# Kernel tuning notes

Measured on AMD Instinct MI355X. Metric: run time of the kernel, lower is better.

The kernel has to match this reference:

```python
import jax, jax.numpy as jnp
import numpy as np

TEMPERATURE = 0.1
NEG_INF = -1e30


def setup_inputs() -> dict:
    key = jax.random.key(0)
    ks = jax.random.split(key, 8)
    T, B, D = 2048, 16, 256
    inp = {
        'q1': jax.random.normal(ks[0], (T, B, D), dtype=jnp.float32),
        'k2': jax.random.normal(ks[1], (T, B, D), dtype=jnp.float32),
        'q2': jax.random.normal(ks[2], (T, B, D), dtype=jnp.float32),
        'k1': jax.random.normal(ks[3], (T, B, D), dtype=jnp.float32),
        'mask_q1': jnp.ones((B, T), dtype=bool),
        'mask_q2': jnp.ones((B, T), dtype=bool),
        'len_q1': jax.random.randint(ks[4], (B,), 0, T, dtype=jnp.int32),
        'len_k2': jax.random.randint(ks[5], (B,), 0, T, dtype=jnp.int32),
        'len_q2': jax.random.randint(ks[6], (B,), 0, T, dtype=jnp.int32),
        'len_k1': jax.random.randint(ks[7], (B,), 0, T, dtype=jnp.int32),
    }
    return inp


def _compute_loss(pred, target, len_pred, len_target):
    # pred, target: (T, B, D) -> (B, T, D)
    pred = jnp.transpose(pred, (1, 0, 2))
    target = jnp.transpose(target, (1, 0, 2))
    B, T, _ = pred.shape
    min_l = jnp.minimum(len_pred, len_target)  # (B,)

    # Batched truncated matmul realized as full matmul + column masking.
    logits = jnp.einsum('btd,bsd->bts', pred, target) / TEMPERATURE  # (B, T, T)
    idx = jnp.arange(T)
    col_valid = idx[None, None, :] < min_l[:, None, None]
    logits = jnp.where(col_valid, logits, NEG_INF)

    # Cross-entropy with labels = arange(min_l): loss_i = lse_i - logits[i, i]
    lse = jax.nn.logsumexp(logits, axis=-1)                 # (B, T)
    diag = jnp.diagonal(logits, axis1=1, axis2=2)           # (B, T)
    row_loss = lse - diag

    row_valid = idx[None, :] < min_l[:, None]               # (B, T)
    denom = jnp.maximum(min_l, 1).astype(pred.dtype)
    per_sample = jnp.sum(jnp.where(row_valid, row_loss, 0.0), axis=1) / denom

    valid = min_l > 0
    n_valid = jnp.sum(valid.astype(pred.dtype))
    total = jnp.sum(jnp.where(valid, per_sample, 0.0))
    return jnp.where(n_valid > 0, total / jnp.maximum(n_valid, 1.0), 0.0)


def reference(q1, k2, q2, k1, mask_q1, mask_q2, len_q1, len_k2, len_q2, len_k1):
    # masks are unused in the original math (kept for interface fidelity)
    loss_a = _compute_loss(q1, k2, len_q1, len_k2)
    loss_b = _compute_loss(q2, k1, len_q2, len_k1)
    return (loss_a + loss_b) / 2
```

## Files before the change

### kernel.cpp

```cpp
#include <hip/hip_runtime.h>
#include <hip/hip_bf16.h>
#include <cmath>

#define T_DIM 2048
#define B_DIM 16
#define D_DIM 256
#define BD (B_DIM * D_DIM)
#define BM 256
#define BN 64
#define NS 4
#define CHUNK (T_DIM / NS)
#define NEG_INF_F (-1e30f)

typedef __attribute__((ext_vector_type(8))) short bf16x8;
typedef __attribute__((ext_vector_type(8))) unsigned short ushort8;
typedef __attribute__((ext_vector_type(4))) float f32x4;

static __device__ __forceinline__ ushort f2bf(float f) {
    union { float f; unsigned int u; } x; x.f = f;
    unsigned int r = (x.u + 0x7FFFu + ((x.u >> 16) & 1u)) >> 16;
    return (ushort)r;
}

static __device__ __forceinline__ void gload_lds16(const ushort* g, ushort* l) {
    __builtin_amdgcn_global_load_lds(
        (const __attribute__((address_space(1))) unsigned int*)g,
        (__attribute__((address_space(3))) unsigned int*)l,
        16, 0, 0);
}

__global__ __launch_bounds__(256) void convert_kernel(
    const float* __restrict__ q1, const float* __restrict__ k2,
    const float* __restrict__ q2, const float* __restrict__ k1,
    const int* __restrict__ lq1, const int* __restrict__ lk2,
    const int* __restrict__ lq2, const int* __restrict__ lk1,
    ushort* __restrict__ wsbf)
{
    const int idx    = blockIdx.x * 256 + threadIdx.x;
    const int tensor = idx >> 20;
    const int rem    = idx & 1048575;
    const int t      = rem >> 9;
    const int r2     = rem & 511;
    const int b      = r2 >> 5;
    const int d8     = (r2 & 31) * 8;
    const int m = (tensor < 2) ? min(lq1[b], lk2[b]) : min(lq2[b], lk1[b]);
    if (t >= m) return;

    const float* src = (tensor == 0) ? q1 : (tensor == 1) ? k2 : (tensor == 2) ? q2 : k1;
    const float scale = (tensor == 0 || tensor == 2) ? 10.0f : 1.0f;
    const size_t off = (size_t)t * BD + (size_t)b * D_DIM + d8;
    const float4 v0 = *reinterpret_cast<const float4*>(&src[off]);
    const float4 v1 = *reinterpret_cast<const float4*>(&src[off + 4]);
    ushort8 h;
    h[0] = f2bf(v0.x * scale); h[1] = f2bf(v0.y * scale);
    h[2] = f2bf(v0.z * scale); h[3] = f2bf(v0.w * scale);
    h[4] = f2bf(v1.x * scale); h[5] = f2bf(v1.y * scale);
    h[6] = f2bf(v1.z * scale); h[7] = f2bf(v1.w * scale);
    const size_t TBD = (size_t)T_DIM * BD;
    ushort* dst = &wsbf[(size_t)tensor * TBD + (size_t)t * BD + (size_t)b * D_DIM
                        + (d8 ^ ((t & 15) << 3))];
    *reinterpret_cast<ushort8*>(dst) = h;
}

__global__ __launch_bounds__(512) void partial_lse_bf_kernel(
    const ushort* __restrict__ wsbf,
    const int* __restrict__ len_q1, const int* __restrict__ len_k2,
    const int* __restrict__ len_q2, const int* __restrict__ len_k1,
    float2* __restrict__ partial, float* __restrict__ diag)
{
    const int pair = blockIdx.z / NS;
    const int sc   = blockIdx.z % NS;
    const int b    = blockIdx.y;
    const int t0   = blockIdx.x * BM;

    const int lp = (pair == 0) ? len_q1[b] : len_q2[b];
    const int lt = (pair == 0) ? len_k2[b] : len_k1[b];
    const int m  = min(lp, lt);
    const int s_start = sc * CHUNK;
    if (t0 >= m || s_start >= m) return;
    const int s_hi = min(m, s_start + CHUNK);
    const int pb = pair * B_DIM + b;

    const size_t TBD = (size_t)T_DIM * BD;
    const ushort* pred = wsbf + (size_t)(pair ? 2 : 0) * TBD;
    const ushort* targ = wsbf + (size_t)(pair ? 3 : 1) * TBD;

    __shared__ ushort tl[2][BN * 256];

    const int tid = threadIdx.x;
    const int w   = tid >> 6;
    const int l   = tid & 63;
    const int c   = l & 15;
    const int g   = l >> 4;

    #pragma unroll
    for (int q = 0; q < 4; ++q) {
        const int r = 8 * w + 2 * q + (l >> 5);
        const ushort* gp = &targ[(size_t)(s_start + r) * BD + (size_t)b * D_DIM + (l & 31) * 8];
        gload_lds16(gp, &tl[0][(4 * w + q) * 512]);
    }

    bf16x8 afrag[2][8];
    #pragma unroll
    for (int i = 0; i < 2; ++i) {
        const ushort* base = &pred[(size_t)(t0 + 32 * w + 16 * i + c) * BD + (size_t)b * D_DIM];
        #pragma unroll
        for (int kk = 0; kk < 8; ++kk) {
            const int d = g * 8 + kk * 32;
            afrag[i][kk] = *reinterpret_cast<const bf16x8*>(&base[d ^ (c << 3)]);
        }
    }

    float tmax[2][4], tsum[2][4], dg[2][4];
    #pragma unroll
    for (int i = 0; i < 2; ++i)
        #pragma unroll
        for (int rr = 0; rr < 4; ++rr) {
            tmax[i][rr] = NEG_INF_F; tsum[i][rr] = 0.0f; dg[i][rr] = NEG_INF_F;
        }

    __syncthreads();
    int cur = 0;

    for (int s0 = s_start; s0 < s_hi; s0 += BN) {
        if (s0 + BN < s_hi) {
            const int nxt = cur ^ 1;
            #pragma unroll
            for (int q = 0; q < 4; ++q) {
                const int r = 8 * w + 2 * q + (l >> 5);
                const ushort* gp = &targ[(size_t)(s0 + BN + r) * BD + (size_t)b * D_DIM + (l & 31) * 8];
                gload_lds16(gp, &tl[nxt][(4 * w + q) * 512]);
            }
        }

        f32x4 acc[2][4];
        #pragma unroll
        for (int i = 0; i < 2; ++i)
            #pragma unroll
            for (int j = 0; j < 4; ++j)
                acc[i][j] = (f32x4){0.f, 0.f, 0.f, 0.f};

        const ushort* buf = tl[cur];
        #pragma unroll
        for (int kk = 0; kk < 8; ++kk) {
            bf16x8 bfrag[4];
            #pragma unroll
            for (int j = 0; j < 4; ++j) {
                const int r = 16 * j + c;
                const int d = g * 8 + kk * 32;
                bfrag[j] = *reinterpret_cast<const bf16x8*>(&buf[(r << 8) + (d ^ (c << 3))]);
            }
            #pragma unroll
            for (int i = 0; i < 2; ++i)
                #pragma unroll
                for (int j = 0; j < 4; ++j)
                    acc[i][j] = __builtin_amdgcn_mfma_f32_16x16x32_bf16(
                        afrag[i][kk], bfrag[j], acc[i][j], 0, 0, 0);
        }

        #pragma unroll
        for (int i = 0; i < 2; ++i) {
            #pragma unroll
            for (int rr = 0; rr < 4; ++rr) {
                const int trow = t0 + 32 * w + 16 * i + 4 * g + rr;
                float lg[4];
                float cmax = NEG_INF_F;
                #pragma unroll
                for (int j = 0; j < 4; ++j) {
                    const int s = s0 + 16 * j + c;
                    float v = acc[i][j][rr];
                    v = (s < m) ? v : NEG_INF_F;
                    if (s == trow) dg[i][rr] = v;
                    lg[j] = v;
                    cmax = fmaxf(cmax, v);
                }
                const float nmax = fmaxf(tmax[i][rr], cmax);
                const float add = __expf(lg[0] - nmax) + __expf(lg[1] - nmax)
                                + __expf(lg[2] - nmax) + __expf(lg[3] - nmax);
                tsum[i][rr] = tsum[i][rr] * __expf(tmax[i][rr] - nmax) + add;
                tmax[i][rr] = nmax;
            }
        }

        __syncthreads();
        cur ^= 1;
    }

    const bool own_diag = (t0 >= s_start) && (t0 + BM <= s_start + CHUNK);
    #pragma unroll
    for (int i = 0; i < 2; ++i) {
        #pragma unroll
        for (int rr = 0; rr < 4; ++rr) {
            float M = tmax[i][rr], S = tsum[i][rr];
            #pragma unroll
            for (int msk = 1; msk < 16; msk <<= 1) {
                const float Mo = __shfl_xor(M, msk, 64);
                const float So = __shfl_xor(S, msk, 64);
                const float nM = fmaxf(M, Mo);
                S = S * __expf(M - nM) + So * __expf(Mo - nM);
                M = nM;
            }
            float d = dg[i][rr];
            #pragma unroll
            for (int msk = 1; msk < 16; msk <<= 1)
                d = fmaxf(d, __shfl_xor(d, msk, 64));
            if (c == 0) {
                const int trow = t0 + 32 * w + 16 * i + 4 * g + rr;
                partial[((size_t)(pb << 11) + trow) * NS + sc] = make_float2(M, S);
                if (own_diag) diag[(pb << 11) + trow] = d;
            }
        }
    }
}

__global__ __launch_bounds__(256) void partial_lse_f32_kernel(
    const float* __restrict__ q1, const float* __restrict__ k2,
    const float* __restrict__ q2, const float* __restrict__ k1,
    const int* __restrict__ len_q1, const int* __restrict__ len_k2,
    const int* __restrict__ len_q2, const int* __restrict__ len_k1,
    float2* __restrict__ partial, float* __restrict__ diag,
    int chunk, int ns)
{
    const int pair = blockIdx.z / ns;
    const int sc   = blockIdx.z % ns;
    const int b    = blockIdx.y;
    const int t0   = blockIdx.x * 128;

    const float* pred = (pair == 0) ? q1 : q2;
    const float* targ = (pair == 0) ? k2 : k1;
    const int lp = (pair == 0) ? len_q1[b] : len_q2[b];
    const int lt = (pair == 0) ? len_k2[b] : len_k1[b];
    const int m  = min(lp, lt);
    const int s_start = sc * chunk;
    if (t0 >= m || s_start >= m) return;
    const int s_hi = min(m, s_start + chunk);
    const int pb = pair * B_DIM + b;

    __shared__ ushort tlf[BN * 256];

    const int tid = threadIdx.x;
    const int w   = tid >> 6;
    const int l   = tid & 63;
    const int c   = l & 15;
    const int g   = l >> 4;

    bf16x8 afrag[2][8];
    #pragma unroll
    for (int i = 0; i < 2; ++i) {
        const float* base = &pred[(size_t)(t0 + 32 * w + 16 * i + c) * BD + (size_t)b * D_DIM];
        #pragma unroll
        for (int kk = 0; kk < 8; ++kk) {
            const int d = g * 8 + kk * 32;
            const float4 v0 = *reinterpret_cast<const float4*>(base + d);
            const float4 v1 = *reinterpret_cast<const float4*>(base + d + 4);
            bf16x8 av;
            av[0] = (short)f2bf(v0.x * 10.f); av[1] = (short)f2bf(v0.y * 10.f);
            av[2] = (short)f2bf(v0.z * 10.f); av[3] = (short)f2bf(v0.w * 10.f);
            av[4] = (short)f2bf(v1.x * 10.f); av[5] = (short)f2bf(v1.y * 10.f);
            av[6] = (short)f2bf(v1.z * 10.f); av[7] = (short)f2bf(v1.w * 10.f);
            afrag[i][kk] = av;
        }
    }

    float tmax[2][4], tsum[2][4], dg[2][4];
    #pragma unroll
    for (int i = 0; i < 2; ++i)
        #pragma unroll
        for (int rr = 0; rr < 4; ++rr) {
            tmax[i][rr] = NEG_INF_F; tsum[i][rr] = 0.0f; dg[i][rr] = NEG_INF_F;
        }

    for (int s0 = s_start; s0 < s_hi; s0 += BN) {
        __syncthreads();
        #pragma unroll
        for (int v = 0; v < 16; ++v) {
            const int f  = v * 256 + tid;
            const int r  = f >> 6;
            const int d0 = (f & 63) * 4;
            const float4 vv = *reinterpret_cast<const float4*>(
                &targ[(size_t)(s0 + r) * BD + (size_t)b * D_DIM + d0]);
            ushort4 h;
            h.x = f2bf(vv.x); h.y = f2bf(vv.y); h.z = f2bf(vv.z); h.w = f2bf(vv.w);
            *reinterpret_cast<ushort4*>(&tlf[(r << 8) + (d0 ^ ((r & 15) << 3))]) = h;
        }
        __syncthreads();

        f32x4 acc[2][4];
        #pragma unroll
        for (int i = 0; i < 2; ++i)
            #pragma unroll
            for (int j = 0; j < 4; ++j)
                acc[i][j] = (f32x4){0.f, 0.f, 0.f, 0.f};

        #pragma unroll
        for (int kk = 0; kk < 8; ++kk) {
            bf16x8 bfrag[4];
            #pragma unroll
            for (int j = 0; j < 4; ++j) {
                const int r = 16 * j + c;
                const int d = g * 8 + kk * 32;
                bfrag[j] = *reinterpret_cast<const bf16x8*>(&tlf[(r << 8) + (d ^ (c << 3))]);
            }
            #pragma unroll
            for (int i = 0; i < 2; ++i)
                #pragma unroll
                for (int j = 0; j < 4; ++j)
                    acc[i][j] = __builtin_amdgcn_mfma_f32_16x16x32_bf16(
                        afrag[i][kk], bfrag[j], acc[i][j], 0, 0, 0);
        }

        #pragma unroll
        for (int i = 0; i < 2; ++i) {
            #pragma unroll
            for (int rr = 0; rr < 4; ++rr) {
                const int trow = t0 + 32 * w + 16 * i + 4 * g + rr;
                float lg[4];
                float cmax = NEG_INF_F;
                #pragma unroll
                for (int j = 0; j < 4; ++j) {
                    const int s = s0 + 16 * j + c;
                    float v = acc[i][j][rr];
                    v = (s < m) ? v : NEG_INF_F;
                    if (s == trow) dg[i][rr] = v;
                    lg[j] = v;
                    cmax = fmaxf(cmax, v);
                }
                const float nmax = fmaxf(tmax[i][rr], cmax);
                const float add = __expf(lg[0] - nmax) + __expf(lg[1] - nmax)
                                + __expf(lg[2] - nmax) + __expf(lg[3] - nmax);
                tsum[i][rr] = tsum[i][rr] * __expf(tmax[i][rr] - nmax) + add;
                tmax[i][rr] = nmax;
            }
        }
    }

    const bool own_diag = (t0 >= s_start) && (t0 + 128 <= s_start + chunk);
    #pragma unroll
    for (int i = 0; i < 2; ++i) {
        #pragma unroll
        for (int rr = 0; rr < 4; ++rr) {
            float M = tmax[i][rr], S = tsum[i][rr];
            #pragma unroll
            for (int msk = 1; msk < 16; msk <<= 1) {
                const float Mo = __shfl_xor(M, msk, 64);
                const float So = __shfl_xor(S, msk, 64);
                const float nM = fmaxf(M, Mo);
                S = S * __expf(M - nM) + So * __expf(Mo - nM);
                M = nM;
            }
            float d = dg[i][rr];
            #pragma unroll
            for (int msk = 1; msk < 16; msk <<= 1)
                d = fmaxf(d, __shfl_xor(d, msk, 64));
            if (c == 0) {
                const int trow = t0 + 32 * w + 16 * i + 4 * g + rr;
                partial[((size_t)(pb << 11) + trow) * ns + sc] = make_float2(M, S);
                if (own_diag) diag[(pb << 11) + trow] = d;
            }
        }
    }
}

__global__ __launch_bounds__(256) void combine_kernel(
    const int* __restrict__ len_q1, const int* __restrict__ len_k2,
    const int* __restrict__ len_q2, const int* __restrict__ len_k1,
    const float2* __restrict__ partial, const float* __restrict__ diag,
    float* __restrict__ per_sample, int chunk, int ns)
{
    const int pb   = blockIdx.x;
    const int pair = pb >> 4;
    const int b    = pb & 15;
    const int lp = (pair == 0) ? len_q1[b] : len_q2[b];
    const int lt = (pair == 0) ? len_k2[b] : len_k1[b];
    const int m  = min(lp, lt);

    float local = 0.0f;
    if (m > 0) {
        const int nch = (m + chunk - 1) / chunk;
        for (int t = threadIdx.x; t < m; t += 256) {
            float M = NEG_INF_F, S = 0.0f;
            for (int sc = 0; sc < nch; ++sc) {
                const float2 p = partial[((size_t)(pb << 11) + t) * ns + sc];
                const float nM = fmaxf(M, p.x);
                S = S * __expf(M - nM) + p.y * __expf(p.x - nM);
                M = nM;
            }
            local += (__logf(S) + M) - diag[(pb << 11) + t];
        }
    }

    __shared__ float ws4[4];
    #pragma unroll
    for (int msk = 1; msk < 64; msk <<= 1)
        local += __shfl_xor(local, msk, 64);
    if ((threadIdx.x & 63) == 0) ws4[threadIdx.x >> 6] = local;
    __syncthreads();
    if (threadIdx.x == 0) {
        const float tot = ws4[0] + ws4[1] + ws4[2] + ws4[3];
        per_sample[pb] = (m > 0) ? (tot / (float)m) : 0.0f;
    }
}

__global__ void finalize_kernel(
    const int* __restrict__ len_q1, const int* __restrict__ len_k2,
    const int* __restrict__ len_q2, const int* __restrict__ len_k1,
    const float* __restrict__ per_sample, float* __restrict__ out)
{
    if (threadIdx.x != 0 || blockIdx.x != 0) return;
    float losses[2];
    #pragma unroll
    for (int p = 0; p < 2; ++p) {
        float tot = 0.0f, nv = 0.0f;
        for (int b = 0; b < B_DIM; ++b) {
            const int lp = (p == 0) ? len_q1[b] : len_q2[b];
            const int lt = (p == 0) ? len_k2[b] : len_k1[b];
            const int mm = min(lp, lt);
            if (mm > 0) { tot += per_sample[p * B_DIM + b]; nv += 1.0f; }
        }
        losses[p] = (nv > 0.0f) ? (tot / nv) : 0.0f;
    }
    out[0] = 0.5f * (losses[0] + losses[1]);
}

extern "C" void kernel_launch(void* const* d_in, const int* in_sizes, int n_in,
                              void* d_out, int out_size, void* d_ws, size_t ws_size,
                              hipStream_t stream) {
    const float* q1 = (const float*)d_in[0];
    const float* k2 = (const float*)d_in[1];
    const float* q2 = (const float*)d_in[2];
    const float* k1 = (const float*)d_in[3];
    const int* lq1 = (const int*)d_in[6];
    const int* lk2 = (const int*)d_in[7];
    const int* lq2 = (const int*)d_in[8];
    const int* lk1 = (const int*)d_in[9];
    float* out = (float*)d_out;

    const size_t TBD  = (size_t)T_DIM * BD;
    const size_t rows = (size_t)2 * B_DIM * T_DIM;
    const size_t bfbytes = 4 * TBD * sizeof(ushort);
    const size_t need_pre = bfbytes + rows * NS * sizeof(float2) + rows * sizeof(float) + 256;

    if (ws_size >= need_pre) {
        ushort* wsbf       = (ushort*)d_ws;
        float2* partial    = (float2*)((char*)d_ws + bfbytes);
        float*  diag       = (float*)((char*)partial + rows * NS * sizeof(float2));
        float*  per_sample = diag + rows;

        convert_kernel<<<16384, 256, 0, stream>>>(q1, k2, q2, k1, lq1, lk2, lq2, lk1, wsbf);

        dim3 gridA(T_DIM / BM, B_DIM, 2 * NS);
        partial_lse_bf_kernel<<<gridA, 512, 0, stream>>>(
            wsbf, lq1, lk2, lq2, lk1, partial, diag);

        combine_kernel<<<32, 256, 0, stream>>>(
            lq1, lk2, lq2, lk1, partial, diag, per_sample, CHUNK, NS);
        finalize_kernel<<<1, 64, 0, stream>>>(lq1, lk2, lq2, lk1, per_sample, out);
    } else {
        int ns = 8;
        while (ns > 1) {
            const size_t need = rows * ns * sizeof(float2) + rows * sizeof(float) + 256;
            if (need <= ws_size) break;
            ns >>= 1;
        }
        const int chunk = T_DIM / ns;
        float2* partial    = (float2*)d_ws;
        float*  diag       = (float*)((char*)d_ws + rows * ns * sizeof(float2));
        float*  per_sample = diag + rows;

        dim3 gridA(T_DIM / 128, B_DIM, 2 * ns);
        partial_lse_f32_kernel<<<gridA, 256, 0, stream>>>(
            q1, k2, q2, k1, lq1, lk2, lq2, lk1, partial, diag, chunk, ns);

        combine_kernel<<<32, 256, 0, stream>>>(
            lq1, lk2, lq2, lk1, partial, diag, per_sample, chunk, ns);
        finalize_kernel<<<1, 64, 0, stream>>>(lq1, lk2, lq2, lk1, per_sample, out);
    }
}
```

Baseline: 77.69 us.

## Restructure bf16 LSE kernel: smaller M tile, 2x2 warp split, triple-buffered LDS, exp2

The bf16 partial-LSE kernel now uses 128-row tiles with eight warps arranged as 4 row groups by 2 column halves. Each warp keeps its own partial (max,sum), so the partial buffer doubles and the combine kernel merges twice as many entries. Pred rows are staged through LDS with direct global-to-LDS loads, and target tiles are triple-buffered with explicit vmcnt waits so two tiles can be in flight. The log2(e)/T factor is folded into the pred conversion so the kernels can use exp2 and log2, at the cost of more partial traffic and a more complex barrier scheme.

```diff
diff --git a/kernel.cpp b/kernel.cpp
--- a/kernel.cpp
+++ b/kernel.cpp
@@ -6,11 +6,13 @@
 #define B_DIM 16
 #define D_DIM 256
 #define BD (B_DIM * D_DIM)
-#define BM 256
-#define BN 64
+#define BMA 128
+#define BNA 64
 #define NS 4
 #define CHUNK (T_DIM / NS)
 #define NEG_INF_F (-1e30f)
+#define SCALE_LOG2 14.4269504088896f
+#define LN2F 0.6931471805599453f
 
 typedef __attribute__((ext_vector_type(8))) short bf16x8;
 typedef __attribute__((ext_vector_type(8))) unsigned short ushort8;
@@ -47,7 +49,7 @@
     if (t >= m) return;
 
     const float* src = (tensor == 0) ? q1 : (tensor == 1) ? k2 : (tensor == 2) ? q2 : k1;
-    const float scale = (tensor == 0 || tensor == 2) ? 10.0f : 1.0f;
+    const float scale = (tensor == 0 || tensor == 2) ? SCALE_LOG2 : 1.0f;
     const size_t off = (size_t)t * BD + (size_t)b * D_DIM + d8;
     const float4 v0 = *reinterpret_cast<const float4*>(&src[off]);
     const float4 v1 = *reinterpret_cast<const float4*>(&src[off + 4]);
@@ -71,7 +73,7 @@
     const int pair = blockIdx.z / NS;
     const int sc   = blockIdx.z % NS;
     const int b    = blockIdx.y;
-    const int t0   = blockIdx.x * BM;
+    const int t0   = blockIdx.x * BMA;
 
     const int lp = (pair == 0) ? len_q1[b] : len_q2[b];
     const int lt = (pair == 0) ? len_k2[b] : len_k1[b];
@@ -85,31 +87,55 @@
     const ushort* pred = wsbf + (size_t)(pair ? 2 : 0) * TBD;
     const ushort* targ = wsbf + (size_t)(pair ? 3 : 1) * TBD;
 
-    __shared__ ushort tl[2][BN * 256];
+    __shared__ ushort tls[3 * BNA * 256];
 
     const int tid = threadIdx.x;
     const int w   = tid >> 6;
     const int l   = tid & 63;
     const int c   = l & 15;
     const int g   = l >> 4;
-
-    #pragma unroll
-    for (int q = 0; q < 4; ++q) {
-        const int r = 8 * w + 2 * q + (l >> 5);
-        const ushort* gp = &targ[(size_t)(s_start + r) * BD + (size_t)b * D_DIM + (l & 31) * 8];
-        gload_lds16(gp, &tl[0][(4 * w + q) * 512]);
-    }
+    const int tg  = w >> 1;
+    const int sh  = w & 1;
+
+    #pragma unroll
+    for (int h = 0; h < 2; ++h)
+        #pragma unroll
+        for (int q = 0; q < 4; ++q) {
+            const int pr = t0 + 64 * h + 8 * w + 2 * q + (l >> 5);
+            gload_lds16(&pred[(size_t)pr * BD + (size_t)b * D_DIM + (l & 31) * 8],
+                        &tls[h * (BNA * 256) + (4 * w + q) * 512]);
+        }
+    asm volatile("s_waitcnt vmcnt(0)" ::: "memory");
+    __builtin_amdgcn_s_barrier();
 
     bf16x8 afrag[2][8];
     #pragma unroll
     for (int i = 0; i < 2; ++i) {
-        const ushort* base = &pred[(size_t)(t0 + 32 * w + 16 * i + c) * BD + (size_t)b * D_DIM];
+        const int ar = 32 * tg + 16 * i + c;
+        const ushort* base = &tls[(ar >> 6) * (BNA * 256) + ((ar & 63) << 8)];
         #pragma unroll
         for (int kk = 0; kk < 8; ++kk) {
             const int d = g * 8 + kk * 32;
             afrag[i][kk] = *reinterpret_cast<const bf16x8*>(&base[d ^ (c << 3)]);
         }
     }
+    __syncthreads();
+
+    const int nstage = (s_hi - s_start + BNA - 1) / BNA;
+    #pragma unroll
+    for (int q = 0; q < 4; ++q) {
+        const int r = 8 * w + 2 * q + (l >> 5);
+        gload_lds16(&targ[(size_t)(s_start + r) * BD + (size_t)b * D_DIM + (l & 31) * 8],
+                    &tls[(4 * w + q) * 512]);
+    }
+    if (nstage > 1) {
+        #pragma unroll
+        for (int q = 0; q < 4; ++q) {
+            const int r = 8 * w + 2 * q + (l >> 5);
+            gload_lds16(&targ[(size_t)(s_start + BNA + r) * BD + (size_t)b * D_DIM + (l & 31) * 8],
+                        &tls[(BNA * 256) + (4 * w + q) * 512]);
+        }
+    }
 
     float tmax[2][4], tsum[2][4], dg[2][4];
     #pragma unroll
@@ -119,19 +145,174 @@
             tmax[i][rr] = NEG_INF_F; tsum[i][rr] = 0.0f; dg[i][rr] = NEG_INF_F;
         }
 
-    __syncthreads();
-    int cur = 0;
-
-    for (int s0 = s_start; s0 < s_hi; s0 += BN) {
-        if (s0 + BN < s_hi) {
-            const int nxt = cur ^ 1;
+    asm volatile("s_waitcnt vmcnt(0)" ::: "memory");
+    __builtin_amdgcn_sched_barrier(0);
+    __builtin_amdgcn_s_barrier();
+    __builtin_amdgcn_sched_barrier(0);
+
+    int cb = 0;
+    for (int st = 0; st < nstage; ++st) {
+        const int s0 = s_start + st * BNA;
+        const bool pf = (st + 2 < nstage);
+        if (pf) {
+            int db = cb - 1; if (db < 0) db = 2;
             #pragma unroll
             for (int q = 0; q < 4; ++q) {
                 const int r = 8 * w + 2 * q + (l >> 5);
-                const ushort* gp = &targ[(size_t)(s0 + BN + r) * BD + (size_t)b * D_DIM + (l & 31) * 8];
-                gload_lds16(gp, &tl[nxt][(4 * w + q) * 512]);
-            }
-        }
+                gload_lds16(&targ[(size_t)(s0 + 2 * BNA + r) * BD + (size_t)b * D_DIM + (l & 31) * 8],
+                            &tls[db * (BNA * 256) + (4 * w + q) * 512]);
+            }
+        }
+
+        const ushort* buf = &tls[cb * (BNA * 256)];
+        f32x4 acc[2][2];
+        #pragma unroll
+        for (int i = 0; i < 2; ++i)
+            #pragma unroll
+            for (int j = 0; j < 2; ++j)
+                acc[i][j] = (f32x4){0.f, 0.f, 0.f, 0.f};
+
+        #pragma unroll
+        for (int kk = 0; kk < 8; ++kk) {
+            bf16x8 bfrag[2];
+            #pragma unroll
+            for (int j = 0; j < 2; ++j) {
+                const int r = 32 * sh + 16 * j + c;
+                const int d = g * 8 + kk * 32;
+                bfrag[j] = *reinterpret_cast<const bf16x8*>(&buf[(r << 8) + (d ^ (c << 3))]);
+            }
+            #pragma unroll
+            for (int i = 0; i < 2; ++i)
+                #pragma unroll
+                for (int j = 0; j < 2; ++j)
+                    acc[i][j] = __builtin_amdgcn_mfma_f32_16x16x32_bf16(
+                        afrag[i][kk], bfrag[j], acc[i][j], 0, 0, 0);
+        }
+
+        #pragma unroll
+        for (int i = 0; i < 2; ++i) {
+            #pragma unroll
+            for (int rr = 0; rr < 4; ++rr) {
+                const int trow = t0 + 32 * tg + 16 * i + 4 * g + rr;
+                const int s0c  = s0 + 32 * sh + c;
+                float v0 = (s0c      < m) ? acc[i][0][rr] : NEG_INF_F;
+                float v1 = (s0c + 16 < m) ? acc[i][1][rr] : NEG_INF_F;
+                if (s0c      == trow) dg[i][rr] = v0;
+                if (s0c + 16 == trow) dg[i][rr] = v1;
+                const float cmax = fmaxf(v0, v1);
+                const float nmax = fmaxf(tmax[i][rr], cmax);
+                const float add  = exp2f(v0 - nmax) + exp2f(v1 - nmax);
+                tsum[i][rr] = tsum[i][rr] * exp2f(tmax[i][rr] - nmax) + add;
+                tmax[i][rr] = nmax;
+            }
+        }
+
+        if (pf) { asm volatile("s_waitcnt vmcnt(4)" ::: "memory"); }
+        else    { asm volatile("s_waitcnt vmcnt(0)" ::: "memory"); }
+        __builtin_amdgcn_sched_barrier(0);
+        __builtin_amdgcn_s_barrier();
+        __builtin_amdgcn_sched_barrier(0);
+        ++cb; if (cb == 3) cb = 0;
+    }
+
+    const bool own_diag = (t0 >= s_start) && (t0 + BMA <= s_start + CHUNK);
+    #pragma unroll
+    for (int i = 0; i < 2; ++i) {
+        #pragma unroll
+        for (int rr = 0; rr < 4; ++rr) {
+            float M = tmax[i][rr], S = tsum[i][rr];
+            #pragma unroll
+            for (int msk = 1; msk < 16; msk <<= 1) {
+                const float Mo = __shfl_xor(M, msk, 64);
+                const float So = __shfl_xor(S, msk, 64);
+                const float nM = fmaxf(M, Mo);
+                S = S * exp2f(M - nM) + So * exp2f(Mo - nM);
+                M = nM;
+            }
+            float d = dg[i][rr];
+            #pragma unroll
+            for (int msk = 1; msk < 16; msk <<= 1)
+                d = fmaxf(d, __shfl_xor(d, msk, 64));
+            if (c == 0) {
+                const int trow = t0 + 32 * tg + 16 * i + 4 * g + rr;
+                partial[((size_t)(pb << 11) + trow) * (2 * NS) + sc * 2 + sh] = make_float2(M, S);
+                if (own_diag && d > -1.0e29f) diag[(pb << 11) + trow] = d;
+            }
+        }
+    }
+}
+
+__global__ __launch_bounds__(256) void partial_lse_f32_kernel(
+    const float* __restrict__ q1, const float* __restrict__ k2,
+    const float* __restrict__ q2, const float* __restrict__ k1,
+    const int* __restrict__ len_q1, const int* __restrict__ len_k2,
+    const int* __restrict__ len_q2, const int* __restrict__ len_k1,
+    float2* __restrict__ partial, float* __restrict__ diag,
+    int chunk, int ns)
+{
+    const int pair = blockIdx.z / ns;
+    const int sc   = blockIdx.z % ns;
+    const int b    = blockIdx.y;
+    const int t0   = blockIdx.x * 128;
+
+    const float* pred = (pair == 0) ? q1 : q2;
+    const float* targ = (pair == 0) ? k2 : k1;
+    const int lp = (pair == 0) ? len_q1[b] : len_q2[b];
+    const int lt = (pair == 0) ? len_k2[b] : len_k1[b];
+    const int m  = min(lp, lt);
+    const int s_start = sc * chunk;
+    if (t0 >= m || s_start >= m) return;
+    const int s_hi = min(m, s_start + chunk);
+    const int pb = pair * B_DIM + b;
+
+    __shared__ ushort tlf[BNA * 256];
+
+    const int tid = threadIdx.x;
+    const int w   = tid >> 6;
+    const int l   = tid & 63;
+    const int c   = l & 15;
+    const int g   = l >> 4;
+
+    bf16x8 afrag[2][8];
+    #pragma unroll
+    for (int i = 0; i < 2; ++i) {
+        const float* base = &pred[(size_t)(t0 + 32 * w + 16 * i + c) * BD + (size_t)b * D_DIM];
+        #pragma unroll
+        for (int kk = 0; kk < 8; ++kk) {
+            const int d = g * 8 + kk * 32;
+            const float4 v0 = *reinterpret_cast<const float4*>(base + d);
+            const float4 v1 = *reinterpret_cast<const float4*>(base + d + 4);
+            bf16x8 av;
+            av[0] = (short)f2bf(v0.x * SCALE_LOG2); av[1] = (short)f2bf(v0.y * SCALE_LOG2);
+            av[2] = (short)f2bf(v0.z * SCALE_LOG2); av[3] = (short)f2bf(v0.w * SCALE_LOG2);
+            av[4] = (short)f2bf(v1.x * SCALE_LOG2); av[5] = (short)f2bf(v1.y * SCALE_LOG2);
+            av[6] = (short)f2bf(v1.z * SCALE_LOG2); av[7] = (short)f2bf(v1.w * SCALE_LOG2);
+            afrag[i][kk] = av;
+        }
+    }
+
+    float tmax[2][4], tsum[2][4], dg[2][4];
+    #pragma unroll
+    for (int i = 0; i < 2; ++i)
+        #pragma unroll
+        for (int rr = 0; rr < 4; ++rr) {
+            tmax[i][rr] = NEG_INF_F; tsum[i][rr] = 0.0f; dg[i][rr] = NEG_INF_F;
+        }
+
+    for (int s0 = s_start; s0 < s_hi; s0 += BNA) {
+        __syncthreads();
+        #pragma unroll
+        for (int v = 0; v < 16; ++v) {
+            const int f  = v * 256 + tid;
+            const int r  = f >> 6;
+            const int d0 = (f & 63) * 4;
+            const float4 vv = *reinterpret_cast<const float4*>(
+                &targ[(size_t)(s0 + r) * BD + (size_t)b * D_DIM + d0]);
+            ushort4 h;
+            h.x = f2bf(vv.x); h.y = f2bf(vv.y); h.z = f2bf(vv.z); h.w = f2bf(vv.w);
+            *reinterpret_cast<ushort4*>(&tlf[(r << 8) + (d0 ^ ((r & 15) << 3))]) = h;
+        }
+        __syncthreads();
 
         f32x4 acc[2][4];
         #pragma unroll
@@ -140,7 +321,6 @@
             for (int j = 0; j < 4; ++j)
                 acc[i][j] = (f32x4){0.f, 0.f, 0.f, 0.f};
 
-        const ushort* buf = tl[cur];
         #pragma unroll
         for (int kk = 0; kk < 8; ++kk) {
             bf16x8 bfrag[4];
@@ -148,7 +328,7 @@
             for (int j = 0; j < 4; ++j) {
                 const int r = 16 * j + c;
                 const int d = g * 8 + kk * 32;
-                bfrag[j] = *reinterpret_cast<const bf16x8*>(&buf[(r << 8) + (d ^ (c << 3))]);
+                bfrag[j] = *reinterpret_cast<const bf16x8*>(&tlf[(r << 8) + (d ^ (c << 3))]);
             }
             #pragma unroll
             for (int i = 0; i < 2; ++i)
@@ -175,18 +355,15 @@
                     cmax = fmaxf(cmax, v);
                 }
                 const float nmax = fmaxf(tmax[i][rr], cmax);
-                const float add = __expf(lg[0] - nmax) + __expf(lg[1] - nmax)
-                                + __expf(lg[2] - nmax) + __expf(lg[3] - nmax);
-                tsum[i][rr] = tsum[i][rr] * __expf(tmax[i][rr] - nmax) + add;
+                const float add = exp2f(lg[0] - nmax) + exp2f(lg[1] - nmax)
+                                + exp2f(lg[2] - nmax) + exp2f(lg[3] - nmax);
+                tsum[i][rr] = tsum[i][rr] * exp2f(tmax[i][rr] - nmax) + add;
                 tmax[i][rr] = nmax;
             }
         }
-
-        __syncthreads();
-        cur ^= 1;
-    }
-
-    const bool own_diag = (t0 >= s_start) && (t0 + BM <= s_start + CHUNK);
+    }
+
+    const bool own_diag = (t0 >= s_start) && (t0 + 128 <= s_start + chunk);
     #pragma unroll
     for (int i = 0; i < 2; ++i) {
         #pragma unroll
@@ -197,155 +374,7 @@
                 const float Mo = __shfl_xor(M, msk, 64);
                 const float So = __shfl_xor(S, msk, 64);
                 const float nM = fmaxf(M, Mo);
-                S = S * __expf(M - nM) + So * __expf(Mo - nM);
-                M = nM;
-            }
-            float d = dg[i][rr];
-            #pragma unroll
-            for (int msk = 1; msk < 16; msk <<= 1)
-                d = fmaxf(d, __shfl_xor(d, msk, 64));
-            if (c == 0) {
-                const int trow = t0 + 32 * w + 16 * i + 4 * g + rr;
-                partial[((size_t)(pb << 11) + trow) * NS + sc] = make_float2(M, S);
-                if (own_diag) diag[(pb << 11) + trow] = d;
-            }
-        }
-    }
-}
-
-__global__ __launch_bounds__(256) void partial_lse_f32_kernel(
-    const float* __restrict__ q1, const float* __restrict__ k2,
-    const float* __restrict__ q2, const float* __restrict__ k1,
-    const int* __restrict__ len_q1, const int* __restrict__ len_k2,
-    const int* __restrict__ len_q2, const int* __restrict__ len_k1,
-    float2* __restrict__ partial, float* __restrict__ diag,
-    int chunk, int ns)
-{
-    const int pair = blockIdx.z / ns;
-    const int sc   = blockIdx.z % ns;
-    const int b    = blockIdx.y;
-    const int t0   = blockIdx.x * 128;
-
-    const float* pred = (pair == 0) ? q1 : q2;
-    const float* targ = (pair == 0) ? k2 : k1;
-    const int lp = (pair == 0) ? len_q1[b] : len_q2[b];
-    const int lt = (pair == 0) ? len_k2[b] : len_k1[b];
-    const int m  = min(lp, lt);
-    const int s_start = sc * chunk;
-    if (t0 >= m || s_start >= m) return;
-    const int s_hi = min(m, s_start + chunk);
-    const int pb = pair * B_DIM + b;
-
-    __shared__ ushort tlf[BN * 256];
-
-    const int tid = threadIdx.x;
-    const int w   = tid >> 6;
-    const int l   = tid & 63;
-    const int c   = l & 15;
-    const int g   = l >> 4;
-
-    bf16x8 afrag[2][8];
-    #pragma unroll
-    for (int i = 0; i < 2; ++i) {
-        const float* base = &pred[(size_t)(t0 + 32 * w + 16 * i + c) * BD + (size_t)b * D_DIM];
-        #pragma unroll
-        for (int kk = 0; kk < 8; ++kk) {
-            const int d = g * 8 + kk * 32;
-            const float4 v0 = *reinterpret_cast<const float4*>(base + d);
-            const float4 v1 = *reinterpret_cast<const float4*>(base + d + 4);
-            bf16x8 av;
-            av[0] = (short)f2bf(v0.x * 10.f); av[1] = (short)f2bf(v0.y * 10.f);
-            av[2] = (short)f2bf(v0.z * 10.f); av[3] = (short)f2bf(v0.w * 10.f);
-            av[4] = (short)f2bf(v1.x * 10.f); av[5] = (short)f2bf(v1.y * 10.f);
-            av[6] = (short)f2bf(v1.z * 10.f); av[7] = (short)f2bf(v1.w * 10.f);
-            afrag[i][kk] = av;
-        }
-    }
-
-    float tmax[2][4], tsum[2][4], dg[2][4];
-    #pragma unroll
-    for (int i = 0; i < 2; ++i)
-        #pragma unroll
-        for (int rr = 0; rr < 4; ++rr) {
-            tmax[i][rr] = NEG_INF_F; tsum[i][rr] = 0.0f; dg[i][rr] = NEG_INF_F;
-        }
-
-    for (int s0 = s_start; s0 < s_hi; s0 += BN) {
-        __syncthreads();
-        #pragma unroll
-        for (int v = 0; v < 16; ++v) {
-            const int f  = v * 256 + tid;
-            const int r  = f >> 6;
-            const int d0 = (f & 63) * 4;
-            const float4 vv = *reinterpret_cast<const float4*>(
-                &targ[(size_t)(s0 + r) * BD + (size_t)b * D_DIM + d0]);
-            ushort4 h;
-            h.x = f2bf(vv.x); h.y = f2bf(vv.y); h.z = f2bf(vv.z); h.w = f2bf(vv.w);
-            *reinterpret_cast<ushort4*>(&tlf[(r << 8) + (d0 ^ ((r & 15) << 3))]) = h;
-        }
-        __syncthreads();
-
-        f32x4 acc[2][4];
-        #pragma unroll
-        for (int i = 0; i < 2; ++i)
-            #pragma unroll
-            for (int j = 0; j < 4; ++j)
-                acc[i][j] = (f32x4){0.f, 0.f, 0.f, 0.f};
-
-        #pragma unroll
-        for (int kk = 0; kk < 8; ++kk) {
-            bf16x8 bfrag[4];
-            #pragma unroll
-            for (int j = 0; j < 4; ++j) {
-                const int r = 16 * j + c;
-                const int d = g * 8 + kk * 32;
-                bfrag[j] = *reinterpret_cast<const bf16x8*>(&tlf[(r << 8) + (d ^ (c << 3))]);
-            }
-            #pragma unroll
-            for (int i = 0; i < 2; ++i)
-                #pragma unroll
-                for (int j = 0; j < 4; ++j)
-                    acc[i][j] = __builtin_amdgcn_mfma_f32_16x16x32_bf16(
-                        afrag[i][kk], bfrag[j], acc[i][j], 0, 0, 0);
-        }
-
-        #pragma unroll
-        for (int i = 0; i < 2; ++i) {
-            #pragma unroll
-            for (int rr = 0; rr < 4; ++rr) {
-                const int trow = t0 + 32 * w + 16 * i + 4 * g + rr;
-                float lg[4];
-                float cmax = NEG_INF_F;
-                #pragma unroll
-                for (int j = 0; j < 4; ++j) {
-                    const int s = s0 + 16 * j + c;
-                    float v = acc[i][j][rr];
-                    v = (s < m) ? v : NEG_INF_F;
-                    if (s == trow) dg[i][rr] = v;
-                    lg[j] = v;
-                    cmax = fmaxf(cmax, v);
-                }
-                const float nmax = fmaxf(tmax[i][rr], cmax);
-                const float add = __expf(lg[0] - nmax) + __expf(lg[1] - nmax)
-                                + __expf(lg[2] - nmax) + __expf(lg[3] - nmax);
-                tsum[i][rr] = tsum[i][rr] * __expf(tmax[i][rr] - nmax) + add;
-                tmax[i][rr] = nmax;
-            }
-        }
-    }
-
-    const bool own_diag = (t0 >= s_start) && (t0 + 128 <= s_start + chunk);
-    #pragma unroll
-    for (int i = 0; i < 2; ++i) {
-        #pragma unroll
-        for (int rr = 0; rr < 4; ++rr) {
-            float M = tmax[i][rr], S = tsum[i][rr];
-            #pragma unroll
-            for (int msk = 1; msk < 16; msk <<= 1) {
-                const float Mo = __shfl_xor(M, msk, 64);
-                const float So = __shfl_xor(S, msk, 64);
-                const float nM = fmaxf(M, Mo);
-                S = S * __expf(M - nM) + So * __expf(Mo - nM);
+                S = S * exp2f(M - nM) + So * exp2f(Mo - nM);
                 M = nM;
             }
             float d = dg[i][rr];
@@ -365,7 +394,7 @@
     const int* __restrict__ len_q1, const int* __restrict__ len_k2,
     const int* __restrict__ len_q2, const int* __restrict__ len_k1,
     const float2* __restrict__ partial, const float* __restrict__ diag,
-    float* __restrict__ per_sample, int chunk, int ns)
+    float* __restrict__ per_sample, int chunk, int stride, int mult)
 {
     const int pb   = blockIdx.x;
     const int pair = pb >> 4;
@@ -376,16 +405,16 @@
 
     float local = 0.0f;
     if (m > 0) {
-        const int nch = (m + chunk - 1) / chunk;
+        const int nch = mult * ((m + chunk - 1) / chunk);
         for (int t = threadIdx.x; t < m; t += 256) {
             float M = NEG_INF_F, S = 0.0f;
-            for (int sc = 0; sc < nch; ++sc) {
-                const float2 p = partial[((size_t)(pb << 11) + t) * ns + sc];
+            for (int e = 0; e < nch; ++e) {
+                const float2 p = partial[((size_t)(pb << 11) + t) * stride + e];
                 const float nM = fmaxf(M, p.x);
-                S = S * __expf(M - nM) + p.y * __expf(p.x - nM);
+                S = S * exp2f(M - nM) + p.y * exp2f(p.x - nM);
                 M = nM;
             }
-            local += (__logf(S) + M) - diag[(pb << 11) + t];
+            local += LN2F * ((__log2f(S) + M) - diag[(pb << 11) + t]);
         }
     }
 
@@ -438,22 +467,23 @@
     const size_t TBD  = (size_t)T_DIM * BD;
     const size_t rows = (size_t)2 * B_DIM * T_DIM;
     const size_t bfbytes = 4 * TBD * sizeof(ushort);
-    const size_t need_pre = bfbytes + rows * NS * sizeof(float2) + rows * sizeof(float) + 256;
+    const size_t pbytes  = rows * (2 * NS) * sizeof(float2);
+    const size_t need_pre = bfbytes + pbytes + rows * sizeof(float) + 256;
 
     if (ws_size >= need_pre) {
         ushort* wsbf       = (ushort*)d_ws;
         float2* partial    = (float2*)((char*)d_ws + bfbytes);
-        float*  diag       = (float*)((char*)partial + rows * NS * sizeof(float2));
+        float*  diag       = (float*)((char*)partial + pbytes);
         float*  per_sample = diag + rows;
 
         convert_kernel<<<16384, 256, 0, stream>>>(q1, k2, q2, k1, lq1, lk2, lq2, lk1, wsbf);
 
-        dim3 gridA(T_DIM / BM, B_DIM, 2 * NS);
+        dim3 gridA(T_DIM / BMA, B_DIM, 2 * NS);
         partial_lse_bf_kernel<<<gridA, 512, 0, stream>>>(
             wsbf, lq1, lk2, lq2, lk1, partial, diag);
 
         combine_kernel<<<32, 256, 0, stream>>>(
-            lq1, lk2, lq2, lk1, partial, diag, per_sample, CHUNK, NS);
+            lq1, lk2, lq2, lk1, partial, diag, per_sample, CHUNK, 2 * NS, 2);
         finalize_kernel<<<1, 64, 0, stream>>>(lq1, lk2, lq2, lk1, per_sample, out);
     } else {
         int ns = 8;
@@ -472,7 +502,7 @@
             q1, k2, q2, k1, lq1, lk2, lq2, lk1, partial, diag, chunk, ns);
 
         combine_kernel<<<32, 256, 0, stream>>>(
-            lq1, lk2, lq2, lk1, partial, diag, per_sample, chunk, ns);
+            lq1, lk2, lq2, lk1, partial, diag, per_sample, chunk, ns, 1);
         finalize_kernel<<<1, 64, 0, stream>>>(lq1, lk2, lq2, lk1, per_sample, out);
     }
 }
```

Result: slower. 105.8 us (+36.1%).

## Relayout bf16 workspace per batch, shrink tiles, stage pred via LDS, use exp2

Applied to the files above, without the earlier changes.

The converted bf16 workspace is now stored per (tensor, batch) as contiguous T x 256 slabs, so each row tile becomes a contiguous range that can be bulk-loaded with global-to-LDS transfers. The pred tile is staged through LDS before fragment extraction, and the target tiles are double-buffered with two preloaded stages. The row tile shrinks from 256 to 128 with 256 threads and the column split grows from 4 to 8 chunks, giving more blocks. The softmax scale now folds in log2(e) so the kernel can use exp2/log2, with a final ln2 rescale in the combine step.

```diff
diff --git a/kernel.cpp b/kernel.cpp
--- a/kernel.cpp
+++ b/kernel.cpp
@@ -6,11 +6,15 @@
 #define B_DIM 16
 #define D_DIM 256
 #define BD (B_DIM * D_DIM)
-#define BM 256
+#define ROWU 256
+#define SLAB (T_DIM * ROWU)
+#define BM 128
 #define BN 64
-#define NS 4
+#define NS 8
 #define CHUNK (T_DIM / NS)
 #define NEG_INF_F (-1e30f)
+#define SCALE_LOG2 14.4269504088896f
+#define LN2F 0.6931471805599453f
 
 typedef __attribute__((ext_vector_type(8))) short bf16x8;
 typedef __attribute__((ext_vector_type(8))) unsigned short ushort8;
@@ -47,7 +51,7 @@
     if (t >= m) return;
 
     const float* src = (tensor == 0) ? q1 : (tensor == 1) ? k2 : (tensor == 2) ? q2 : k1;
-    const float scale = (tensor == 0 || tensor == 2) ? 10.0f : 1.0f;
+    const float scale = (tensor == 0 || tensor == 2) ? SCALE_LOG2 : 1.0f;
     const size_t off = (size_t)t * BD + (size_t)b * D_DIM + d8;
     const float4 v0 = *reinterpret_cast<const float4*>(&src[off]);
     const float4 v1 = *reinterpret_cast<const float4*>(&src[off + 4]);
@@ -56,13 +60,12 @@
     h[2] = f2bf(v0.z * scale); h[3] = f2bf(v0.w * scale);
     h[4] = f2bf(v1.x * scale); h[5] = f2bf(v1.y * scale);
     h[6] = f2bf(v1.z * scale); h[7] = f2bf(v1.w * scale);
-    const size_t TBD = (size_t)T_DIM * BD;
-    ushort* dst = &wsbf[(size_t)tensor * TBD + (size_t)t * BD + (size_t)b * D_DIM
+    ushort* dst = &wsbf[(size_t)(tensor * B_DIM + b) * SLAB + (size_t)t * ROWU
                         + (d8 ^ ((t & 15) << 3))];
     *reinterpret_cast<ushort8*>(dst) = h;
 }
 
-__global__ __launch_bounds__(512) void partial_lse_bf_kernel(
+__global__ __launch_bounds__(256) void partial_lse_bf_kernel(
     const ushort* __restrict__ wsbf,
     const int* __restrict__ len_q1, const int* __restrict__ len_k2,
     const int* __restrict__ len_q2, const int* __restrict__ len_k1,
@@ -81,11 +84,10 @@
     const int s_hi = min(m, s_start + CHUNK);
     const int pb = pair * B_DIM + b;
 
-    const size_t TBD = (size_t)T_DIM * BD;
-    const ushort* pred = wsbf + (size_t)(pair ? 2 : 0) * TBD;
-    const ushort* targ = wsbf + (size_t)(pair ? 3 : 1) * TBD;
-
-    __shared__ ushort tl[2][BN * 256];
+    const ushort* pred = wsbf + (size_t)((pair ? 2 : 0) * B_DIM + b) * SLAB;
+    const ushort* targ = wsbf + (size_t)((pair ? 3 : 1) * B_DIM + b) * SLAB;
+
+    __shared__ ushort tls[2 * BN * ROWU];
 
     const int tid = threadIdx.x;
     const int w   = tid >> 6;
@@ -94,20 +96,38 @@
     const int g   = l >> 4;
 
     #pragma unroll
-    for (int q = 0; q < 4; ++q) {
-        const int r = 8 * w + 2 * q + (l >> 5);
-        const ushort* gp = &targ[(size_t)(s_start + r) * BD + (size_t)b * D_DIM + (l & 31) * 8];
-        gload_lds16(gp, &tl[0][(4 * w + q) * 512]);
-    }
+    for (int q = 0; q < 16; ++q) {
+        const int chunk16 = q * 4 + w;
+        gload_lds16(&pred[(size_t)t0 * ROWU + chunk16 * 512 + l * 8],
+                    &tls[chunk16 * 512]);
+    }
+    __syncthreads();
 
     bf16x8 afrag[2][8];
     #pragma unroll
     for (int i = 0; i < 2; ++i) {
-        const ushort* base = &pred[(size_t)(t0 + 32 * w + 16 * i + c) * BD + (size_t)b * D_DIM];
+        const int ar = 32 * w + 16 * i + c;
         #pragma unroll
         for (int kk = 0; kk < 8; ++kk) {
             const int d = g * 8 + kk * 32;
-            afrag[i][kk] = *reinterpret_cast<const bf16x8*>(&base[d ^ (c << 3)]);
+            afrag[i][kk] = *reinterpret_cast<const bf16x8*>(&tls[(ar << 8) + (d ^ (c << 3))]);
+        }
+    }
+    __syncthreads();
+
+    const int nstage = (s_hi - s_start + BN - 1) / BN;
+    #pragma unroll
+    for (int q = 0; q < 8; ++q) {
+        const int chunk16 = q * 4 + w;
+        gload_lds16(&targ[(size_t)s_start * ROWU + chunk16 * 512 + l * 8],
+                    &tls[chunk16 * 512]);
+    }
+    if (nstage > 1) {
+        #pragma unroll
+        for (int q = 0; q < 8; ++q) {
+            const int chunk16 = q * 4 + w;
+            gload_lds16(&targ[(size_t)(s_start + BN) * ROWU + chunk16 * 512 + l * 8],
+                        &tls[BN * ROWU + chunk16 * 512]);
         }
     }
 
@@ -122,17 +142,21 @@
     __syncthreads();
     int cur = 0;
 
-    for (int s0 = s_start; s0 < s_hi; s0 += BN) {
-        if (s0 + BN < s_hi) {
+    for (int st = 0; st < nstage; ++st) {
+        const int s0 = s_start + st * BN;
+        if (st + 2 < nstage + 1 && st + 1 < nstage && st >= 1) {  }
+
+        if (st >= 1 && st + 1 < nstage) {
             const int nxt = cur ^ 1;
             #pragma unroll
-            for (int q = 0; q < 4; ++q) {
-                const int r = 8 * w + 2 * q + (l >> 5);
-                const ushort* gp = &targ[(size_t)(s0 + BN + r) * BD + (size_t)b * D_DIM + (l & 31) * 8];
-                gload_lds16(gp, &tl[nxt][(4 * w + q) * 512]);
-            }
-        }
-
+            for (int q = 0; q < 8; ++q) {
+                const int chunk16 = q * 4 + w;
+                gload_lds16(&targ[(size_t)(s0 + BN) * ROWU + chunk16 * 512 + l * 8],
+                            &tls[nxt * (BN * ROWU) + chunk16 * 512]);
+            }
+        }
+
+        const ushort* buf = &tls[cur * (BN * ROWU)];
         f32x4 acc[2][4];
         #pragma unroll
         for (int i = 0; i < 2; ++i)
@@ -140,7 +164,6 @@
             for (int j = 0; j < 4; ++j)
                 acc[i][j] = (f32x4){0.f, 0.f, 0.f, 0.f};
 
-        const ushort* buf = tl[cur];
         #pragma unroll
         for (int kk = 0; kk < 8; ++kk) {
             bf16x8 bfrag[4];
@@ -175,9 +198,9 @@
                     cmax = fmaxf(cmax, v);
                 }
                 const float nmax = fmaxf(tmax[i][rr], cmax);
-                const float add = __expf(lg[0] - nmax) + __expf(lg[1] - nmax)
-                                + __expf(lg[2] - nmax) + __expf(lg[3] - nmax);
-                tsum[i][rr] = tsum[i][rr] * __expf(tmax[i][rr] - nmax) + add;
+                const float add = exp2f(lg[0] - nmax) + exp2f(lg[1] - nmax)
+                                + exp2f(lg[2] - nmax) + exp2f(lg[3] - nmax);
+                tsum[i][rr] = tsum[i][rr] * exp2f(tmax[i][rr] - nmax) + add;
                 tmax[i][rr] = nmax;
             }
         }
@@ -197,7 +220,7 @@
                 const float Mo = __shfl_xor(M, msk, 64);
                 const float So = __shfl_xor(S, msk, 64);
                 const float nM = fmaxf(M, Mo);
-                S = S * __expf(M - nM) + So * __expf(Mo - nM);
+                S = S * exp2f(M - nM) + So * exp2f(Mo - nM);
                 M = nM;
             }
             float d = dg[i][rr];
@@ -254,10 +277,10 @@
             const float4 v0 = *reinterpret_cast<const float4*>(base + d);
             const float4 v1 = *reinterpret_cast<const float4*>(base + d + 4);
             bf16x8 av;
-            av[0] = (short)f2bf(v0.x * 10.f); av[1] = (short)f2bf(v0.y * 10.f);
-            av[2] = (short)f2bf(v0.z * 10.f); av[3] = (short)f2bf(v0.w * 10.f);
-            av[4] = (short)f2bf(v1.x * 10.f); av[5] = (short)f2bf(v1.y * 10.f);
-            av[6] = (short)f2bf(v1.z * 10.f); av[7] = (short)f2bf(v1.w * 10.f);
+            av[0] = (short)f2bf(v0.x * SCALE_LOG2); av[1] = (short)f2bf(v0.y * SCALE_LOG2);
+            av[2] = (short)f2bf(v0.z * SCALE_LOG2); av[3] = (short)f2bf(v0.w * SCALE_LOG2);
+            av[4] = (short)f2bf(v1.x * SCALE_LOG2); av[5] = (short)f2bf(v1.y * SCALE_LOG2);
+            av[6] = (short)f2bf(v1.z * SCALE_LOG2); av[7] = (short)f2bf(v1.w * SCALE_LOG2);
             afrag[i][kk] = av;
         }
     }
@@ -326,9 +349,9 @@
                     cmax = fmaxf(cmax, v);
                 }
                 const float nmax = fmaxf(tmax[i][rr], cmax);
-                const float add = __expf(lg[0] - nmax) + __expf(lg[1] - nmax)
-                                + __expf(lg[2] - nmax) + __expf(lg[3] - nmax);
-                tsum[i][rr] = tsum[i][rr] * __expf(tmax[i][rr] - nmax) + add;
+                const float add = exp2f(lg[0] - nmax) + exp2f(lg[1] - nmax)
+                                + exp2f(lg[2] - nmax) + exp2f(lg[3] - nmax);
+                tsum[i][rr] = tsum[i][rr] * exp2f(tmax[i][rr] - nmax) + add;
                 tmax[i][rr] = nmax;
             }
         }
@@ -345,7 +368,7 @@
                 const float Mo = __shfl_xor(M, msk, 64);
                 const float So = __shfl_xor(S, msk, 64);
                 const float nM = fmaxf(M, Mo);
-                S = S * __expf(M - nM) + So * __expf(Mo - nM);
+                S = S * exp2f(M - nM) + So * exp2f(Mo - nM);
                 M = nM;
             }
             float d = dg[i][rr];
@@ -365,7 +388,7 @@
     const int* __restrict__ len_q1, const int* __restrict__ len_k2,
     const int* __restrict__ len_q2, const int* __restrict__ len_k1,
     const float2* __restrict__ partial, const float* __restrict__ diag,
-    float* __restrict__ per_sample, int chunk, int ns)
+    float* __restrict__ per_sample, int chunk, int stride)
 {
     const int pb   = blockIdx.x;
     const int pair = pb >> 4;
@@ -379,13 +402,13 @@
         const int nch = (m + chunk - 1) / chunk;
         for (int t = threadIdx.x; t < m; t += 256) {
             float M = NEG_INF_F, S = 0.0f;
-            for (int sc = 0; sc < nch; ++sc) {
-                const float2 p = partial[((size_t)(pb << 11) + t) * ns + sc];
+            for (int e = 0; e < nch; ++e) {
+                const float2 p = partial[((size_t)(pb << 11) + t) * stride + e];
                 const float nM = fmaxf(M, p.x);
-                S = S * __expf(M - nM) + p.y * __expf(p.x - nM);
+                S = S * exp2f(M - nM) + p.y * exp2f(p.x - nM);
                 M = nM;
             }
-            local += (__logf(S) + M) - diag[(pb << 11) + t];
+            local += LN2F * ((__log2f(S) + M) - diag[(pb << 11) + t]);
         }
     }
 
@@ -435,21 +458,21 @@
     const int* lk1 = (const int*)d_in[9];
     float* out = (float*)d_out;
 
-    const size_t TBD  = (size_t)T_DIM * BD;
     const size_t rows = (size_t)2 * B_DIM * T_DIM;
-    const size_t bfbytes = 4 * TBD * sizeof(ushort);
-    const size_t need_pre = bfbytes + rows * NS * sizeof(float2) + rows * sizeof(float) + 256;
+    const size_t bfbytes = (size_t)4 * B_DIM * SLAB * sizeof(ushort);
+    const size_t pbytes  = rows * NS * sizeof(float2);
+    const size_t need_pre = bfbytes + pbytes + rows * sizeof(float) + 256;
 
     if (ws_size >= need_pre) {
         ushort* wsbf       = (ushort*)d_ws;
         float2* partial    = (float2*)((char*)d_ws + bfbytes);
-        float*  diag       = (float*)((char*)partial + rows * NS * sizeof(float2));
+        float*  diag       = (float*)((char*)partial + pbytes);
         float*  per_sample = diag + rows;
 
         convert_kernel<<<16384, 256, 0, stream>>>(q1, k2, q2, k1, lq1, lk2, lq2, lk1, wsbf);
 
         dim3 gridA(T_DIM / BM, B_DIM, 2 * NS);
-        partial_lse_bf_kernel<<<gridA, 512, 0, stream>>>(
+        partial_lse_bf_kernel<<<gridA, 256, 0, stream>>>(
             wsbf, lq1, lk2, lq2, lk1, partial, diag);
 
         combine_kernel<<<32, 256, 0, stream>>>(
```

Result: slower. 90.12 us (+16.0%).
